# Kernel tuning notes

Measured on AMD Instinct MI355X. Metric: run time of the kernel, lower is better.

Reference implementation:

```python
import jax, jax.numpy as jnp
import numpy as np


def setup_inputs() -> dict:
    key0 = jax.random.key(0)
    kq, kk, kv = jax.random.split(key0, 3)
    B, S, H, KVH, D = 1, 4096, 8, 2, 64
    return {
        "query": jax.random.normal(kq, (B, S, H, D), dtype=jnp.float32),
        "key": jax.random.normal(kk, (B, S, KVH, D), dtype=jnp.float32),
        "value": jax.random.normal(kv, (B, S, KVH, D), dtype=jnp.float32),
    }


def _ring_attn_single(query, key, value):
    # world_size == 1 (dist uninitialized): ring loop is a single local step
    # with query_offset == key_offset == 0.
    B, S, H, D = query.shape
    KVH = key.shape[2]
    scale = D ** -0.5
    # [B, H, S, D]
    q = query.transpose(0, 2, 1, 3)
    k = key.transpose(0, 2, 1, 3)
    v = value.transpose(0, 2, 1, 3)
    if KVH != H:
        rep = H // KVH
        k = jnp.repeat(k, rep, axis=1)  # repeat_interleave on head dim
        v = jnp.repeat(v, rep, axis=1)
    logits = jnp.einsum("bhqd,bhkd->bhqk", q, k) * scale
    pos = jnp.arange(S)
    causal = pos[:, None] < pos[None, :]  # mask future keys
    logits = jnp.where(causal[None, None], -jnp.inf, logits)
    w = jax.nn.softmax(logits, axis=-1)  # [B, H, S, S]
    attn_out = jnp.einsum("bhqk,bhkd->bhqd", w, v)
    cw = jnp.sum(w, axis=-1, keepdims=True)  # chunk softmax mass (== 1)
    out = attn_out * cw / (cw + 1e-8)  # weight-accumulation renorm
    return out.transpose(0, 2, 1, 3)  # [B, S, H, D]


def reference(query, key, value):
    return _ring_attn_single(query, key, value)
```

## Files before the change

kernel.cpp:

```cpp
#include <hip/hip_runtime.h>
#include <hip/hip_bf16.h>


#define S_LEN 4096
#define H_Q   8
#define H_KV  2
#define DH    64
#define BN    64
#define PITCH 72
#define NEG_BIG (-1e30f)
#define CS (0.125f * 1.44269504088896340736f)

#define CHUNK 6
#define NTR   187
#define KB_SH (S_LEN * H_KV * DH)
#define OB_SH    ((size_t)NTR * H_Q * 128 * DH)
#define L_FLOATS ((size_t)NTR * H_Q * 128)
#define WS_NEED ((size_t)(2 * KB_SH) * 2 + OB_SH * 2 + L_FLOATS * 4)

typedef __attribute__((ext_vector_type(8))) short bf16x8;
typedef __attribute__((ext_vector_type(4))) short s16x4;
typedef __attribute__((ext_vector_type(4))) float f32x4;
typedef __attribute__((ext_vector_type(4))) unsigned int u32x4;

__device__ __forceinline__ short bf(float x) {
    return __builtin_bit_cast(short, __float2bfloat16(x));
}
__device__ __forceinline__ float fbf(short u) {
    return __builtin_bit_cast(float, ((unsigned int)(unsigned short)u) << 16);
}
__device__ __forceinline__ unsigned int cvtpk(float lo, float hi) {
    unsigned int r;
    asm("v_cvt_pk_bf16_f32 %0, %1, %2" : "=v"(r) : "v"(lo), "v"(hi));
    return r;
}

__global__ __launch_bounds__(256)
void ring_attn_prepass(const float* __restrict__ K, const float* __restrict__ V,
                       short* __restrict__ Kb, short* __restrict__ Vt) {
    const int b = blockIdx.x;
    const int t = threadIdx.x;
    if (b < 512) {
        const int i = (b * 256 + t) * 4;
        float4 kv = *(const float4*)(K + i);
        *(unsigned int*)(Kb + i)     = cvtpk(kv.x, kv.y);
        *(unsigned int*)(Kb + i + 2) = cvtpk(kv.z, kv.w);
    } else {
        __shared__ short T[DH * PITCH];
        const int bb  = b - 512;
        const int kvh = bb >> 6;
        const int s0  = (bb & 63) * 64;
        {
            const int r  = t >> 2;
            const int dq = (t & 3) * 16;
            const float* vp = V + ((s0 + r) * H_KV + kvh) * DH + dq;
            float4 a0 = *(const float4*)(vp);
            float4 a1 = *(const float4*)(vp + 4);
            float4 a2 = *(const float4*)(vp + 8);
            float4 a3 = *(const float4*)(vp + 12);
            float e[16] = {a0.x,a0.y,a0.z,a0.w, a1.x,a1.y,a1.z,a1.w,
                           a2.x,a2.y,a2.z,a2.w, a3.x,a3.y,a3.z,a3.w};
#pragma unroll
            for (int i = 0; i < 16; ++i)
                T[(dq + i) * PITCH + r] = bf(e[i]);
        }
        __syncthreads();
        {
            const int d = t >> 2;
            const int q = t & 3;
            s16x4 g0 = *(const s16x4*)(&T[d * PITCH + 4 * q]);
            s16x4 g1 = *(const s16x4*)(&T[d * PITCH + 16 + 4 * q]);
            s16x4 g2 = *(const s16x4*)(&T[d * PITCH + 32 + 4 * q]);
            s16x4 g3 = *(const s16x4*)(&T[d * PITCH + 48 + 4 * q]);
            bf16x8 x0 = bf16x8{g0[0],g0[1],g0[2],g0[3], g1[0],g1[1],g1[2],g1[3]};
            bf16x8 x1 = bf16x8{g2[0],g2[1],g2[2],g2[3], g3[0],g3[1],g3[2],g3[3]};
            short* op = Vt + (kvh * DH + d) * S_LEN + s0 + 16 * q;
            *(bf16x8*)(op)     = x0;
            *(bf16x8*)(op + 8) = x1;
        }
    }
}

template <bool SPLIT>
__global__ __launch_bounds__(256, 4)
void ring_attn_fwd(const float* __restrict__ Q, const short* __restrict__ Kb,
                   const short* __restrict__ Vt, float* __restrict__ O,
                   short* __restrict__ Obuf, float* __restrict__ Lbuf) {
    const int bid = blockIdx.x;
    const int h   = bid & 7;
    int qt, nch, jbeg, jend, tr0;
    if (SPLIT) {
        const int tr = (NTR - 1) - (bid >> 3);
        int g = 0, base = 0;
        for (;;) {
            const int cnt2 = ((g == 10) ? 2 : 3) * (g + 1);
            if (tr < base + cnt2) break;
            base += cnt2; ++g;
        }
        const int u  = tr - base;
        const int qq = u / (g + 1);
        const int ch = u - qq * (g + 1);
        qt   = 3 * g + qq;
        nch  = g + 1;
        tr0  = base + qq * (g + 1);
        jbeg = ch * CHUNK;
        jend = min(2 * qt + 2, jbeg + CHUNK);
    } else {
        qt = 31 - (bid >> 3);
        nch = 1; jbeg = 0; jend = 2 * qt + 2; tr0 = 0;
    }
    const int kvh = h >> 2;

    __shared__ short Ks[BN * PITCH];
    __shared__ short Vs[DH * PITCH];

    const int tid  = threadIdx.x;
    const int w    = tid >> 6;
    const int lane = tid & 63;
    const int c    = lane & 15;
    const int q    = lane >> 4;

    bf16x8 qf[2][2];
#pragma unroll
    for (int st = 0; st < 2; ++st) {
        const int qg = qt * 128 + st * 64 + w * 16 + c;
        const float* qp = Q + (qg * H_Q + h) * DH + q * 8;
        float4 a0 = *(const float4*)(qp);
        float4 a1 = *(const float4*)(qp + 4);
        float4 b0 = *(const float4*)(qp + 32);
        float4 b1 = *(const float4*)(qp + 36);
        u32x4 u0 = {cvtpk(a0.x*CS, a0.y*CS), cvtpk(a0.z*CS, a0.w*CS),
                    cvtpk(a1.x*CS, a1.y*CS), cvtpk(a1.z*CS, a1.w*CS)};
        u32x4 u1 = {cvtpk(b0.x*CS, b0.y*CS), cvtpk(b0.z*CS, b0.w*CS),
                    cvtpk(b1.x*CS, b1.y*CS), cvtpk(b1.z*CS, b1.w*CS)};
        qf[st][0] = __builtin_bit_cast(bf16x8, u0);
        qf[st][1] = __builtin_bit_cast(bf16x8, u1);
    }

    f32x4 acc[2][4] = {};
    float l_lane[2] = {0.f, 0.f};

    const int rr = tid >> 3;
    const int cc = (tid & 7) * 8;

    const int kstep = BN * H_KV * DH;
    const short* kp0 = Kb + (((jbeg * BN) + rr) * H_KV + kvh) * DH + cc;
    const short* kp1 = kp0 + 32 * H_KV * DH;
    const short* vp0 = Vt + (kvh * DH + rr) * S_LEN + jbeg * BN + cc;
    const short* vp1 = vp0 + 32 * S_LEN;
    bf16x8 kr0 = *(const bf16x8*)kp0;
    bf16x8 kr1 = *(const bf16x8*)kp1;
    bf16x8 vr0 = *(const bf16x8*)vp0;
    bf16x8 vr1 = *(const bf16x8*)vp1;

    for (int j = jbeg; j < jend; ++j) {
        __syncthreads();
        *(bf16x8*)(&Ks[rr * PITCH + cc])        = kr0;
        *(bf16x8*)(&Ks[(32 + rr) * PITCH + cc]) = kr1;
        *(bf16x8*)(&Vs[rr * PITCH + cc])        = vr0;
        *(bf16x8*)(&Vs[(32 + rr) * PITCH + cc]) = vr1;
        if (j + 1 < jend) {
            kp0 += kstep; kp1 += kstep; vp0 += BN; vp1 += BN;
            kr0 = *(const bf16x8*)kp0;
            kr1 = *(const bf16x8*)kp1;
            vr0 = *(const bf16x8*)vp0;
            vr1 = *(const bf16x8*)vp1;
        }
        __syncthreads();

        bf16x8 pf[2][2];
#pragma unroll
        for (int st = 0; st < 2; ++st) {
            f32x4 s[4] = {};
#pragma unroll
            for (int nt = 0; nt < 4; ++nt) {
                bf16x8 kf0 = *(const bf16x8*)(&Ks[(nt * 16 + c) * PITCH + q * 8]);
                bf16x8 kf1 = *(const bf16x8*)(&Ks[(nt * 16 + c) * PITCH + q * 8 + 32]);
                s[nt] = __builtin_amdgcn_mfma_f32_16x16x32_bf16(kf0, qf[st][0], s[nt], 0, 0, 0);
                s[nt] = __builtin_amdgcn_mfma_f32_16x16x32_bf16(kf1, qf[st][1], s[nt], 0, 0, 0);
            }
            if (j >= 2 * qt + st) {
                const int koff = (j - 2 * qt - st) * 64;
                const int qrl  = w * 16 + c;
#pragma unroll
                for (int nt = 0; nt < 4; ++nt) {
                    const int kl = koff + nt * 16 + q * 4;
#pragma unroll
                    for (int r = 0; r < 4; ++r)
                        if (kl + r > qrl) s[nt][r] = NEG_BIG;
                }
            }
#pragma unroll
            for (int nt = 0; nt < 4; ++nt)
#pragma unroll
                for (int r = 0; r < 4; ++r) {
                    const float p = __builtin_amdgcn_exp2f(s[nt][r]);
                    s[nt][r] = p;
                    l_lane[st] += p;
                }
            u32x4 w0 = {cvtpk(s[0][0], s[0][1]), cvtpk(s[0][2], s[0][3]),
                        cvtpk(s[1][0], s[1][1]), cvtpk(s[1][2], s[1][3])};
            u32x4 w1 = {cvtpk(s[2][0], s[2][1]), cvtpk(s[2][2], s[2][3]),
                        cvtpk(s[3][0], s[3][1]), cvtpk(s[3][2], s[3][3])};
            pf[st][0] = __builtin_bit_cast(bf16x8, w0);
            pf[st][1] = __builtin_bit_cast(bf16x8, w1);
        }

#pragma unroll
        for (int dt = 0; dt < 4; ++dt) {
            const int base2 = (dt * 16 + c) * PITCH + 16 * q;
            bf16x8 vf0 = *(const bf16x8*)(&Vs[base2]);
            bf16x8 vf1 = *(const bf16x8*)(&Vs[base2 + 8]);
            acc[0][dt] = __builtin_amdgcn_mfma_f32_16x16x32_bf16(pf[0][0], vf0, acc[0][dt], 0, 0, 0);
            acc[0][dt] = __builtin_amdgcn_mfma_f32_16x16x32_bf16(pf[0][1], vf1, acc[0][dt], 0, 0, 0);
            acc[1][dt] = __builtin_amdgcn_mfma_f32_16x16x32_bf16(pf[1][0], vf0, acc[1][dt], 0, 0, 0);
            acc[1][dt] = __builtin_amdgcn_mfma_f32_16x16x32_bf16(pf[1][1], vf1, acc[1][dt], 0, 0, 0);
        }
    }

    float lr[2][4];
#pragma unroll
    for (int st = 0; st < 2; ++st) {
        float t2 = l_lane[st];
        t2 += __shfl_xor(t2, 16);
        t2 += __shfl_xor(t2, 32);
        l_lane[st] = t2;
#pragma unroll
        for (int r = 0; r < 4; ++r)
            lr[st][r] = __shfl(t2, q * 4 + r);
    }

    if (!SPLIT || nch == 1) {
#pragma unroll
        for (int st = 0; st < 2; ++st)
#pragma unroll
            for (int r = 0; r < 4; ++r) {
                const float inv = 1.0f / lr[st][r];
                const int row = qt * 128 + st * 64 + w * 16 + q * 4 + r;
                float* op = O + (row * H_Q + h) * DH + c;
#pragma unroll
                for (int dt = 0; dt < 4; ++dt)
                    op[dt * 16] = acc[st][dt][r] * inv;
            }
    } else {
        const int slot = (tr0 + jbeg / CHUNK) * 8 + h;
        short* ob = Obuf + (size_t)slot * (128 * DH);
#pragma unroll
        for (int st = 0; st < 2; ++st) {
#pragma unroll
            for (int r = 0; r < 4; ++r) {
                const int rin = st * 64 + w * 16 + q * 4 + r;
#pragma unroll
                for (int dt = 0; dt < 4; ++dt)
                    ob[rin * DH + dt * 16 + c] = bf(acc[st][dt][r]);
            }
            if (lane < 16)
                Lbuf[slot * 128 + st * 64 + w * 16 + lane] = l_lane[st];
        }
    }
}

__global__ __launch_bounds__(256)
void ring_attn_combine(const short* __restrict__ Obuf, const float* __restrict__ Lbuf,
                       float* __restrict__ O) {
    const int gid  = blockIdx.x * 256 + threadIdx.x;
    const int d    = gid & 63;
    const int h    = (gid >> 6) & 7;
    const int srow = 384 + (gid >> 9);
    const int qt   = srow >> 7;
    const int rin  = srow & 127;
    const int g    = qt / 3;
    const int base = 3 * g * (g + 1) / 2;
    const int nch  = g + 1;
    const int tr0  = base + (qt - 3 * g) * nch;

    float num = 0.0f, den = 0.0f;
    for (int ch = 0; ch < nch; ++ch) {
        const int slot = (tr0 + ch) * 8 + h;
        den += Lbuf[slot * 128 + rin];
        num += fbf(Obuf[(size_t)slot * (128 * DH) + rin * DH + d]);
    }
    O[(srow * H_Q + h) * DH + d] = num / den;
}

extern "C" void kernel_launch(void* const* d_in, const int* in_sizes, int n_in,
                              void* d_out, int out_size, void* d_ws, size_t ws_size,
                              hipStream_t stream) {
    const float* Q = (const float*)d_in[0];
    const float* K = (const float*)d_in[1];
    const float* V = (const float*)d_in[2];
    float* O  = (float*)d_out;
    short* Kb = (short*)d_ws;
    short* Vt = Kb + KB_SH;
    short* Obuf = Vt + KB_SH;
    float* Lbuf = (float*)(Obuf + OB_SH);

    ring_attn_prepass<<<640, 256, 0, stream>>>(K, V, Kb, Vt);
    if (ws_size >= WS_NEED) {
        ring_attn_fwd<true><<<NTR * H_Q, 256, 0, stream>>>(Q, Kb, Vt, O, Obuf, Lbuf);
        ring_attn_combine<<<(S_LEN - 384) * H_Q * DH / 256, 256, 0, stream>>>(Obuf, Lbuf, O);
    } else {
        ring_attn_fwd<false><<<32 * H_Q, 256, 0, stream>>>(Q, Kb, Vt, O, Obuf, Lbuf);
    }
}
```

Before: 112.8 us.

## Double-buffer K/V tiles via direct global-to-LDS loads with swizzled layout

The prepass now writes bf16 K and transposed V as contiguous 64x64 tiles with an XOR swizzle on 16-byte chunks. The attention kernel stages each tile straight into double-buffered LDS with global_load_lds, which drops the register round trip and one of the two barriers per iteration. It also reuses each K fragment read for both query sub-tiles. The swizzle is meant to avoid LDS bank conflicts without the padded pitch. The cost is doubled LDS per block, which may cut occupancy, and correctness relies on the barrier waiting for the async LDS loads to finish.

```diff
diff --git a/kernel.cpp b/kernel.cpp
--- a/kernel.cpp
+++ b/kernel.cpp
@@ -7,13 +7,14 @@
 #define H_KV  2
 #define DH    64
 #define BN    64
-#define PITCH 72
 #define NEG_BIG (-1e30f)
 #define CS (0.125f * 1.44269504088896340736f)
 
 #define CHUNK 6
 #define NTR   187
 #define KB_SH (S_LEN * H_KV * DH)
+#define TILE_SH 4096
+#define KVH_SH  (S_LEN * DH)
 #define OB_SH    ((size_t)NTR * H_Q * 128 * DH)
 #define L_FLOATS ((size_t)NTR * H_Q * 128)
 #define WS_NEED ((size_t)(2 * KB_SH) * 2 + OB_SH * 2 + L_FLOATS * 4)
@@ -33,6 +34,11 @@
     unsigned int r;
     asm("v_cvt_pk_bf16_f32 %0, %1, %2" : "=v"(r) : "v"(lo), "v"(hi));
     return r;
+}
+__device__ __forceinline__ void gload16(const short* gp, short* lp) {
+    __builtin_amdgcn_global_load_lds(
+        (const __attribute__((address_space(1))) unsigned int*)gp,
+        (__attribute__((address_space(3))) unsigned int*)lp, 16, 0, 0);
 }
 
 __global__ __launch_bounds__(256)
@@ -42,14 +48,20 @@
     const int t = threadIdx.x;
     if (b < 512) {
         const int i = (b * 256 + t) * 4;
+        const int s   = i >> 7;
+        const int kvh = (i >> 6) & 1;
+        const int d   = i & 63;
         float4 kv = *(const float4*)(K + i);
-        *(unsigned int*)(Kb + i)     = cvtpk(kv.x, kv.y);
-        *(unsigned int*)(Kb + i + 2) = cvtpk(kv.z, kv.w);
+        const int dst = kvh * KVH_SH + (s >> 6) * TILE_SH + (s & 63) * 64
+                      + (((d >> 3) ^ (s & 7)) * 8) + (d & 7);
+        *(unsigned int*)(Kb + dst)     = cvtpk(kv.x, kv.y);
+        *(unsigned int*)(Kb + dst + 2) = cvtpk(kv.z, kv.w);
     } else {
-        __shared__ short T[DH * PITCH];
+        __shared__ short T[DH * 72];
         const int bb  = b - 512;
         const int kvh = bb >> 6;
-        const int s0  = (bb & 63) * 64;
+        const int j   = bb & 63;
+        const int s0  = j * 64;
         {
             const int r  = t >> 2;
             const int dq = (t & 3) * 16;
@@ -61,22 +73,22 @@
             float e[16] = {a0.x,a0.y,a0.z,a0.w, a1.x,a1.y,a1.z,a1.w,
                            a2.x,a2.y,a2.z,a2.w, a3.x,a3.y,a3.z,a3.w};
 #pragma unroll
-            for (int i = 0; i < 16; ++i)
-                T[(dq + i) * PITCH + r] = bf(e[i]);
+            for (int i2 = 0; i2 < 16; ++i2)
+                T[(dq + i2) * 72 + r] = bf(e[i2]);
         }
         __syncthreads();
         {
             const int d = t >> 2;
             const int q = t & 3;
-            s16x4 g0 = *(const s16x4*)(&T[d * PITCH + 4 * q]);
-            s16x4 g1 = *(const s16x4*)(&T[d * PITCH + 16 + 4 * q]);
-            s16x4 g2 = *(const s16x4*)(&T[d * PITCH + 32 + 4 * q]);
-            s16x4 g3 = *(const s16x4*)(&T[d * PITCH + 48 + 4 * q]);
+            s16x4 g0 = *(const s16x4*)(&T[d * 72 + 4 * q]);
+            s16x4 g1 = *(const s16x4*)(&T[d * 72 + 16 + 4 * q]);
+            s16x4 g2 = *(const s16x4*)(&T[d * 72 + 32 + 4 * q]);
+            s16x4 g3 = *(const s16x4*)(&T[d * 72 + 48 + 4 * q]);
             bf16x8 x0 = bf16x8{g0[0],g0[1],g0[2],g0[3], g1[0],g1[1],g1[2],g1[3]};
             bf16x8 x1 = bf16x8{g2[0],g2[1],g2[2],g2[3], g3[0],g3[1],g3[2],g3[3]};
-            short* op = Vt + (kvh * DH + d) * S_LEN + s0 + 16 * q;
-            *(bf16x8*)(op)     = x0;
-            *(bf16x8*)(op + 8) = x1;
+            short* base = Vt + kvh * KVH_SH + j * TILE_SH + d * 64;
+            *(bf16x8*)(base + ((2 * q)     ^ (d & 7)) * 8) = x0;
+            *(bf16x8*)(base + ((2 * q + 1) ^ (d & 7)) * 8) = x1;
         }
     }
 }
@@ -111,14 +123,15 @@
     }
     const int kvh = h >> 2;
 
-    __shared__ short Ks[BN * PITCH];
-    __shared__ short Vs[DH * PITCH];
+    __shared__ short Ksb[2][4096];
+    __shared__ short Vsb[2][4096];
 
     const int tid  = threadIdx.x;
     const int w    = tid >> 6;
     const int lane = tid & 63;
     const int c    = lane & 15;
     const int q    = lane >> 4;
+    const int e    = c & 7;
 
     bf16x8 qf[2][2];
 #pragma unroll
@@ -140,45 +153,44 @@
     f32x4 acc[2][4] = {};
     float l_lane[2] = {0.f, 0.f};
 
-    const int rr = tid >> 3;
-    const int cc = (tid & 7) * 8;
-
-    const int kstep = BN * H_KV * DH;
-    const short* kp0 = Kb + (((jbeg * BN) + rr) * H_KV + kvh) * DH + cc;
-    const short* kp1 = kp0 + 32 * H_KV * DH;
-    const short* vp0 = Vt + (kvh * DH + rr) * S_LEN + jbeg * BN + cc;
-    const short* vp1 = vp0 + 32 * S_LEN;
-    bf16x8 kr0 = *(const bf16x8*)kp0;
-    bf16x8 kr1 = *(const bf16x8*)kp1;
-    bf16x8 vr0 = *(const bf16x8*)vp0;
-    bf16x8 vr1 = *(const bf16x8*)vp1;
+    const short* gkb = Kb + kvh * KVH_SH + w * 1024 + lane * 8;
+    const short* gvb = Vt + kvh * KVH_SH + w * 1024 + lane * 8;
+#define STAGE(buf, j)                                             \
+    do {                                                          \
+        const short* gk = gkb + (j) * TILE_SH;                    \
+        const short* gv = gvb + (j) * TILE_SH;                    \
+        short* lk = &Ksb[buf][w * 1024];                          \
+        short* lv = &Vsb[buf][w * 1024];                          \
+        gload16(gk, lk);        gload16(gk + 512, lk + 512);      \
+        gload16(gv, lv);        gload16(gv + 512, lv + 512);      \
+    } while (0)
+
+    STAGE(0, jbeg);
 
     for (int j = jbeg; j < jend; ++j) {
+        const int cur = (j - jbeg) & 1;
         __syncthreads();
-        *(bf16x8*)(&Ks[rr * PITCH + cc])        = kr0;
-        *(bf16x8*)(&Ks[(32 + rr) * PITCH + cc]) = kr1;
-        *(bf16x8*)(&Vs[rr * PITCH + cc])        = vr0;
-        *(bf16x8*)(&Vs[(32 + rr) * PITCH + cc]) = vr1;
-        if (j + 1 < jend) {
-            kp0 += kstep; kp1 += kstep; vp0 += BN; vp1 += BN;
-            kr0 = *(const bf16x8*)kp0;
-            kr1 = *(const bf16x8*)kp1;
-            vr0 = *(const bf16x8*)vp0;
-            vr1 = *(const bf16x8*)vp1;
-        }
-        __syncthreads();
+        if (j + 1 < jend)
+            STAGE(cur ^ 1, j + 1);
+
+        const short* Kc = Ksb[cur];
+        const short* Vc = Vsb[cur];
+
+        f32x4 s[2][4] = {};
+#pragma unroll
+        for (int nt = 0; nt < 4; ++nt) {
+            const int rb = (nt * 16 + c) * 64;
+            bf16x8 kf0 = *(const bf16x8*)(Kc + rb + (q ^ e) * 8);
+            bf16x8 kf1 = *(const bf16x8*)(Kc + rb + ((q + 4) ^ e) * 8);
+            s[0][nt] = __builtin_amdgcn_mfma_f32_16x16x32_bf16(kf0, qf[0][0], s[0][nt], 0, 0, 0);
+            s[0][nt] = __builtin_amdgcn_mfma_f32_16x16x32_bf16(kf1, qf[0][1], s[0][nt], 0, 0, 0);
+            s[1][nt] = __builtin_amdgcn_mfma_f32_16x16x32_bf16(kf0, qf[1][0], s[1][nt], 0, 0, 0);
+            s[1][nt] = __builtin_amdgcn_mfma_f32_16x16x32_bf16(kf1, qf[1][1], s[1][nt], 0, 0, 0);
+        }
 
         bf16x8 pf[2][2];
 #pragma unroll
         for (int st = 0; st < 2; ++st) {
-            f32x4 s[4] = {};
-#pragma unroll
-            for (int nt = 0; nt < 4; ++nt) {
-                bf16x8 kf0 = *(const bf16x8*)(&Ks[(nt * 16 + c) * PITCH + q * 8]);
-                bf16x8 kf1 = *(const bf16x8*)(&Ks[(nt * 16 + c) * PITCH + q * 8 + 32]);
-                s[nt] = __builtin_amdgcn_mfma_f32_16x16x32_bf16(kf0, qf[st][0], s[nt], 0, 0, 0);
-                s[nt] = __builtin_amdgcn_mfma_f32_16x16x32_bf16(kf1, qf[st][1], s[nt], 0, 0, 0);
-            }
             if (j >= 2 * qt + st) {
                 const int koff = (j - 2 * qt - st) * 64;
                 const int qrl  = w * 16 + c;
@@ -187,30 +199,30 @@
                     const int kl = koff + nt * 16 + q * 4;
 #pragma unroll
                     for (int r = 0; r < 4; ++r)
-                        if (kl + r > qrl) s[nt][r] = NEG_BIG;
+                        if (kl + r > qrl) s[st][nt][r] = NEG_BIG;
                 }
             }
 #pragma unroll
             for (int nt = 0; nt < 4; ++nt)
 #pragma unroll
                 for (int r = 0; r < 4; ++r) {
-                    const float p = __builtin_amdgcn_exp2f(s[nt][r]);
-                    s[nt][r] = p;
+                    const float p = __builtin_amdgcn_exp2f(s[st][nt][r]);
+                    s[st][nt][r] = p;
                     l_lane[st] += p;
                 }
-            u32x4 w0 = {cvtpk(s[0][0], s[0][1]), cvtpk(s[0][2], s[0][3]),
-                        cvtpk(s[1][0], s[1][1]), cvtpk(s[1][2], s[1][3])};
-            u32x4 w1 = {cvtpk(s[2][0], s[2][1]), cvtpk(s[2][2], s[2][3]),
-                        cvtpk(s[3][0], s[3][1]), cvtpk(s[3][2], s[3][3])};
+            u32x4 w0 = {cvtpk(s[st][0][0], s[st][0][1]), cvtpk(s[st][0][2], s[st][0][3]),
+                        cvtpk(s[st][1][0], s[st][1][1]), cvtpk(s[st][1][2], s[st][1][3])};
+            u32x4 w1 = {cvtpk(s[st][2][0], s[st][2][1]), cvtpk(s[st][2][2], s[st][2][3]),
+                        cvtpk(s[st][3][0], s[st][3][1]), cvtpk(s[st][3][2], s[st][3][3])};
             pf[st][0] = __builtin_bit_cast(bf16x8, w0);
             pf[st][1] = __builtin_bit_cast(bf16x8, w1);
         }
 
 #pragma unroll
         for (int dt = 0; dt < 4; ++dt) {
-            const int base2 = (dt * 16 + c) * PITCH + 16 * q;
-            bf16x8 vf0 = *(const bf16x8*)(&Vs[base2]);
-            bf16x8 vf1 = *(const bf16x8*)(&Vs[base2 + 8]);
+            const int nb = (dt * 16 + c) * 64;
+            bf16x8 vf0 = *(const bf16x8*)(Vc + nb + ((2 * q)     ^ e) * 8);
+            bf16x8 vf1 = *(const bf16x8*)(Vc + nb + ((2 * q + 1) ^ e) * 8);
             acc[0][dt] = __builtin_amdgcn_mfma_f32_16x16x32_bf16(pf[0][0], vf0, acc[0][dt], 0, 0, 0);
             acc[0][dt] = __builtin_amdgcn_mfma_f32_16x16x32_bf16(pf[0][1], vf1, acc[0][dt], 0, 0, 0);
             acc[1][dt] = __builtin_amdgcn_mfma_f32_16x16x32_bf16(pf[1][0], vf0, acc[1][dt], 0, 0, 0);
```

Measured after the change: 105.0 us. 1.07x faster.
